# Kernel optimization log

Measured on AMD Instinct MI355X. Metric: run time of the kernel, lower is better.

The kernel has to match this reference:

```python
import jax, jax.numpy as jnp
import numpy as np

T, B, D_IN, NHID = 4096, 8, 512, 512

def setup_inputs() -> dict:
    key = jax.random.key(0)
    k1, k2, k3 = jax.random.split(key, 3)
    scale_i = 1.0 / np.sqrt(D_IN)
    scale_h = 1.0 / np.sqrt(NHID)
    x = jax.random.normal(k1, (T, B, D_IN), dtype=jnp.float32)
    hidden0 = jnp.zeros((2, B, NHID), dtype=jnp.float32)  # [h; cell]
    Wi = jax.random.normal(k2, (D_IN, 4 * NHID), dtype=jnp.float32) * scale_i
    bi = jnp.zeros((4 * NHID,), dtype=jnp.float32)
    Wh = jax.random.normal(k3, (NHID, 4 * NHID), dtype=jnp.float32) * scale_h
    bh = jnp.zeros((4 * NHID,), dtype=jnp.float32)
    return {"x": x, "hidden0": hidden0, "Wi": Wi, "bi": bi, "Wh": Wh, "bh": bh}

def reference(x, hidden0, Wi, bi, Wh, bh):
    n = Wh.shape[0]

    def update(state, xt):
        h, cell = state[0], state[1]               # [B, n] each
        pre = xt @ Wi + bi + h @ Wh + bh           # [B, 4n]
        gates = jax.nn.sigmoid(pre[:, : 3 * n])
        forget_gate = gates[:, :n]
        input_gate = gates[:, n : 2 * n]
        output_gate = gates[:, 2 * n : 3 * n]
        new_cell = jnp.tanh(pre[:, 3 * n :])
        cell = forget_gate * cell + input_gate * new_cell
        h = output_gate * jnp.tanh(cell)
        return jnp.stack([h, cell]), h

    new_state, hidden_stacked = jax.lax.scan(update, hidden0, x)
    return hidden_stacked, new_state
```

## Files before the change

### kernel.cpp

```cpp
#include <hip/hip_runtime.h>
#include <hip/hip_bf16.h>

#define T_STEPS 4096
#define BATCH 8
#define DIN 512
#define NH 512
#define G4 2048
#define NWV 32
#define JPW 16

typedef __attribute__((ext_vector_type(8))) short bf16x8;
typedef __attribute__((ext_vector_type(4))) float f32x4;
typedef __attribute__((ext_vector_type(4))) int i32x4;

__device__ __forceinline__ unsigned short f2b(float f) {
  __hip_bfloat16 h = __float2bfloat16(f);
  return __builtin_bit_cast(unsigned short, h);
}
__device__ __forceinline__ float b2f(unsigned short u) {
  unsigned int x = ((unsigned int)u) << 16;
  return __builtin_bit_cast(float, x);
}
__device__ __forceinline__ float sigf(float x) { return 1.f / (1.f + __expf(-x)); }
__device__ __forceinline__ float tanh_fast(float x) { return 1.f - 2.f / (1.f + __expf(2.f * x)); }

__global__ __launch_bounds__(512) void init_ws(const float* __restrict__ h0,
                                               unsigned int* __restrict__ tags,
                                               unsigned short* __restrict__ hbuf) {
  int tid = threadIdx.x;
  if (tid < NWV) tags[tid] = 0u;
  for (int i = tid; i < 4096; i += 512) {
    int b = i >> 9, j = i & 511;
    hbuf[i] = f2b(h0[b * NH + j]);
    hbuf[4096 + i] = 0;
  }
}

#define BM 64
#define BN 64
#define BK 16
__global__ __launch_bounds__(256) void xi_gemm(const float* __restrict__ x,
                                               const float* __restrict__ Wi,
                                               const float* __restrict__ bi,
                                               const float* __restrict__ bh,
                                               unsigned short* __restrict__ xi) {
  __shared__ float As[BK][BM + 4];
  __shared__ float Bs[BK][BN + 4];
  const int tid = threadIdx.x;
  const int m0 = blockIdx.x * BM;
  const int n0 = blockIdx.y * BN;
  const int tx = tid & 15, ty = tid >> 4;
  const int arow = tid & 63, ak = (tid >> 6) << 2;
  const int bk = tid >> 4, bn = (tid & 15) << 2;
  float acc[4][4] = {};
  for (int k0 = 0; k0 < DIN; k0 += BK) {
    float4 av = *(const float4*)(x + (size_t)(m0 + arow) * DIN + k0 + ak);
    float4 bv = *(const float4*)(Wi + (size_t)(k0 + bk) * G4 + n0 + bn);
    __syncthreads();
    As[ak + 0][arow] = av.x;
    As[ak + 1][arow] = av.y;
    As[ak + 2][arow] = av.z;
    As[ak + 3][arow] = av.w;
    *(float4*)&Bs[bk][bn] = bv;
    __syncthreads();
#pragma unroll
    for (int kk = 0; kk < BK; ++kk) {
      float am[4], bw[4];
      *(float4*)am = *(const float4*)&As[kk][ty << 2];
      *(float4*)bw = *(const float4*)&Bs[kk][tx << 2];
#pragma unroll
      for (int i = 0; i < 4; ++i)
#pragma unroll
        for (int j = 0; j < 4; ++j) acc[i][j] = fmaf(am[i], bw[j], acc[i][j]);
    }
  }
  const int m_base = m0 + (ty << 2);
  const int n_base = n0 + (tx << 2);
  const int tt = m_base >> 3;
  const int rg = (m_base & 7) >> 2;
  const int gate = n_base >> 9;
  const int wv = (n_base & 511) >> 4;
  const int col0 = n_base & 15;
#pragma unroll
  for (int j = 0; j < 4; ++j) {
    int n = n_base + j;
    float bs = bi[n] + bh[n];
    unsigned long long pk = 0;
#pragma unroll
    for (int i = 0; i < 4; ++i)
      pk |= (unsigned long long)f2b(acc[i][j] + bs) << (16 * i);
    int lane = rg * 16 + col0 + j;
    size_t u16idx = (((size_t)tt * NWV + wv) * 32 + lane) * 16 + gate * 4;
    *(unsigned long long*)(xi + u16idx) = pk;
  }
}

__global__ __launch_bounds__(64, 1) void lstm_rec(const float* __restrict__ Wh,
                                                  const float* __restrict__ h0c0,
                                                  const unsigned short* __restrict__ xi,
                                                  float* __restrict__ out,
                                                  unsigned int* tags,
                                                  unsigned short* hbuf) {
  const int wv = blockIdx.x;
  const int j0 = wv * JPW;
  const int lane = threadIdx.x;
  const int col = lane & 15;
  const int rg = lane >> 4;

  __shared__ bf16x8 bwS[4][16][64];

  {
    const int gp = lane >> 4, cp = lane & 15;
    const float* wsrc = Wh + (size_t)gp * NH + j0 + cp;
#pragma unroll 4
    for (int k = 0; k < 512; ++k) {
      float wval = wsrc[(size_t)k * G4];
      const int ks = k >> 5, kq = (k >> 3) & 3, e = k & 7;
      ((unsigned short*)&bwS[gp][ks][kq * 16 + cp])[e] = f2b(wval);
    }
  }
  __syncthreads();

  bf16x8 bwR0[16], bwR1[16];
#pragma unroll
  for (int ks = 0; ks < 16; ++ks) {
    bwR0[ks] = bwS[0][ks][lane];
    bwR1[ks] = bwS[1][ks][lane];
  }

  f32x4 cell = {0.f, 0.f, 0.f, 0.f};
  if (lane < 32) {
#pragma unroll
    for (int q = 0; q < 4; ++q)
      cell[q] = h0c0[(size_t)(BATCH + rg * 4 + q) * NH + j0 + col];
  }

  i32x4 xiC0, xiC1, xiN0, xiN1;
  {
    const unsigned short* xp = xi + ((size_t)wv * 32 + (lane & 31)) * 16;
    asm volatile("global_load_dwordx4 %0, %1, off" : "=&v"(xiC0) : "v"(xp));
    asm volatile("global_load_dwordx4 %0, %1, off offset:16" : "=&v"(xiC1) : "v"(xp));
  }
  f32x4 hq = {0.f, 0.f, 0.f, 0.f};

  const unsigned int* tp = tags + (lane & 31);
  unsigned int* myTag = tags + wv;

  for (int t = 0; t < T_STEPS; ++t) {
    {
      unsigned int tv;
      do {
        asm volatile("global_load_dword %0, %1, off sc1\n\ts_waitcnt vmcnt(0)"
                     : "=v"(tv) : "v"(tp) : "memory");
      } while (__any((int)tv < t));
    }

    const unsigned short* mb = hbuf + ((t & 1) << 12);
    const unsigned short* ap = mb + (col & 7) * 512 + (rg << 3);
    i32x4 afr[16];
    asm volatile("global_load_dwordx4 %0, %1, off sc1" : "=v"(afr[0]) : "v"(ap));
    asm volatile("global_load_dwordx4 %0, %1, off offset:64 sc1" : "=v"(afr[1]) : "v"(ap));
    asm volatile("global_load_dwordx4 %0, %1, off offset:128 sc1" : "=v"(afr[2]) : "v"(ap));
    asm volatile("global_load_dwordx4 %0, %1, off offset:192 sc1" : "=v"(afr[3]) : "v"(ap));
    asm volatile("global_load_dwordx4 %0, %1, off offset:256 sc1" : "=v"(afr[4]) : "v"(ap));
    asm volatile("global_load_dwordx4 %0, %1, off offset:320 sc1" : "=v"(afr[5]) : "v"(ap));
    asm volatile("global_load_dwordx4 %0, %1, off offset:384 sc1" : "=v"(afr[6]) : "v"(ap));
    asm volatile("global_load_dwordx4 %0, %1, off offset:448 sc1" : "=v"(afr[7]) : "v"(ap));
    asm volatile("global_load_dwordx4 %0, %1, off offset:512 sc1" : "=v"(afr[8]) : "v"(ap));
    asm volatile("global_load_dwordx4 %0, %1, off offset:576 sc1" : "=v"(afr[9]) : "v"(ap));
    asm volatile("global_load_dwordx4 %0, %1, off offset:640 sc1" : "=v"(afr[10]) : "v"(ap));
    asm volatile("global_load_dwordx4 %0, %1, off offset:704 sc1" : "=v"(afr[11]) : "v"(ap));
    asm volatile("global_load_dwordx4 %0, %1, off offset:768 sc1" : "=v"(afr[12]) : "v"(ap));
    asm volatile("global_load_dwordx4 %0, %1, off offset:832 sc1" : "=v"(afr[13]) : "v"(ap));
    asm volatile("global_load_dwordx4 %0, %1, off offset:896 sc1" : "=v"(afr[14]) : "v"(ap));
    asm volatile("global_load_dwordx4 %0, %1, off offset:960 sc1" : "=v"(afr[15]) : "v"(ap));
    asm volatile("s_waitcnt vmcnt(0)" ::: "memory");
    __builtin_amdgcn_sched_barrier(0);

    f32x4 acc[4][2];
    {
      unsigned int wrd[8] = {(unsigned int)xiC0[0], (unsigned int)xiC0[1],
                             (unsigned int)xiC0[2], (unsigned int)xiC0[3],
                             (unsigned int)xiC1[0], (unsigned int)xiC1[1],
                             (unsigned int)xiC1[2], (unsigned int)xiC1[3]};
      f32x4 z = {0.f, 0.f, 0.f, 0.f};
#pragma unroll
      for (int g = 0; g < 4; ++g) {
#pragma unroll
        for (int q = 0; q < 4; ++q) {
          const int idx = g * 4 + q;
          acc[g][0][q] = b2f((unsigned short)(wrd[idx >> 1] >> ((idx & 1) * 16)));
        }
        acc[g][1] = z;
      }
    }
#pragma unroll
    for (int ks = 0; ks < 16; ++ks) {
      bf16x8 a = __builtin_bit_cast(bf16x8, afr[ks]);
      acc[0][ks & 1] = __builtin_amdgcn_mfma_f32_16x16x32_bf16(a, bwR0[ks], acc[0][ks & 1], 0, 0, 0);
      acc[1][ks & 1] = __builtin_amdgcn_mfma_f32_16x16x32_bf16(a, bwR1[ks], acc[1][ks & 1], 0, 0, 0);
      acc[2][ks & 1] = __builtin_amdgcn_mfma_f32_16x16x32_bf16(a, bwS[2][ks][lane], acc[2][ks & 1], 0, 0, 0);
      acc[3][ks & 1] = __builtin_amdgcn_mfma_f32_16x16x32_bf16(a, bwS[3][ks][lane], acc[3][ks & 1], 0, 0, 0);
    }

#pragma unroll
    for (int q = 0; q < 4; ++q) {
      float pf = acc[0][0][q] + acc[0][1][q];
      float pi = acc[1][0][q] + acc[1][1][q];
      float po = acc[2][0][q] + acc[2][1][q];
      float pg = acc[3][0][q] + acc[3][1][q];
      float fg = sigf(pf), ig = sigf(pi), og = sigf(po), gg = tanh_fast(pg);
      float cn = fg * cell[q] + ig * gg;
      cell[q] = cn;
      hq[q] = og * tanh_fast(cn);
    }

    if (lane < 32) {
      unsigned short* pp = hbuf + (((t + 1) & 1) << 12) + (rg * 4) * 512 + j0 + col;
      unsigned int h0u = f2b(hq[0]), h1u = f2b(hq[1]), h2u = f2b(hq[2]), h3u = f2b(hq[3]);
      asm volatile("global_store_short %0, %1, off sc1" :: "v"(pp), "v"(h0u) : "memory");
      asm volatile("global_store_short %0, %1, off offset:1024 sc1" :: "v"(pp), "v"(h1u) : "memory");
      asm volatile("global_store_short %0, %1, off offset:2048 sc1" :: "v"(pp), "v"(h2u) : "memory");
      asm volatile("global_store_short %0, %1, off offset:3072 sc1" :: "v"(pp), "v"(h3u) : "memory");
    }
    asm volatile("s_waitcnt vmcnt(0)" ::: "memory");
    if (lane == 0) {
      unsigned int tn1 = (unsigned int)(t + 1);
      asm volatile("global_store_dword %0, %1, off sc1" :: "v"(myTag), "v"(tn1) : "memory");
    }

    if (lane < 32) {
#pragma unroll
      for (int q = 0; q < 4; ++q)
        out[((size_t)t * BATCH + (rg * 4 + q)) * NH + j0 + col] = hq[q];
    }
    {
      const int tn = (t + 1 < T_STEPS) ? (t + 1) : t;
      const unsigned short* xp = xi + (((size_t)tn * NWV + wv) * 32 + (lane & 31)) * 16;
      asm volatile("global_load_dwordx4 %0, %1, off" : "=&v"(xiN0) : "v"(xp));
      asm volatile("global_load_dwordx4 %0, %1, off offset:16" : "=&v"(xiN1) : "v"(xp));
    }
    xiC0 = xiN0;
    xiC1 = xiN1;
  }

  if (lane < 32) {
    const size_t tail = (size_t)T_STEPS * BATCH * NH;
#pragma unroll
    for (int q = 0; q < 4; ++q) {
      out[tail + (size_t)(rg * 4 + q) * NH + j0 + col] = hq[q];
      out[tail + (size_t)BATCH * NH + (size_t)(rg * 4 + q) * NH + j0 + col] = cell[q];
    }
  }
}

extern "C" void kernel_launch(void* const* d_in, const int* in_sizes, int n_in,
                              void* d_out, int out_size, void* d_ws, size_t ws_size,
                              hipStream_t stream) {
  const float* x  = (const float*)d_in[0];
  const float* h0 = (const float*)d_in[1];
  const float* Wi = (const float*)d_in[2];
  const float* bi = (const float*)d_in[3];
  const float* Wh = (const float*)d_in[4];
  const float* bh = (const float*)d_in[5];
  float* out = (float*)d_out;

  unsigned int* tags = (unsigned int*)d_ws;
  unsigned short* hbuf = (unsigned short*)((char*)d_ws + 256);
  unsigned short* xi = (unsigned short*)((char*)d_ws + 65536);

  init_ws<<<1, 512, 0, stream>>>(h0, tags, hbuf);
  dim3 g1((T_STEPS * BATCH) / BM, G4 / BN);
  xi_gemm<<<g1, 256, 0, stream>>>(x, Wi, bi, bh, xi);
  lstm_rec<<<NWV, 64, 0, stream>>>(Wh, h0, xi, out, tags, hbuf);
}
```

Before: 15.11 ms.

## Pipeline tag polling and overlap h-fragment loads with MFMA chunks

The spin-wait on per-wave step tags now keeps two loads in flight and waits with vmcnt(1), so each poll round trip overlaps the next. The accumulator init from precomputed input projections moves ahead of the h loads. The 16 h-fragment loads are consumed in four groups with staggered vmcnt waits, so MFMAs on the first fragments start while later loads are still arriving. This targets per-step latency on the serial recurrence, at the cost of more outstanding polling traffic and a slightly later view of tag updates.

```diff
diff --git a/kernel.cpp b/kernel.cpp
--- a/kernel.cpp
+++ b/kernel.cpp
@@ -148,11 +148,38 @@
 
   for (int t = 0; t < T_STEPS; ++t) {
     {
-      unsigned int tv;
-      do {
-        asm volatile("global_load_dword %0, %1, off sc1\n\ts_waitcnt vmcnt(0)"
-                     : "=v"(tv) : "v"(tp) : "memory");
-      } while (__any((int)tv < t));
+      unsigned int tvA, tvB;
+      asm volatile("global_load_dword %0, %1, off sc1" : "=&v"(tvA) : "v"(tp) : "memory");
+      for (;;) {
+        asm volatile("global_load_dword %0, %1, off sc1" : "=&v"(tvB) : "v"(tp) : "memory");
+        asm volatile("s_waitcnt vmcnt(1)" ::: "memory");
+        __builtin_amdgcn_sched_barrier(0);
+        if (__all((int)tvA >= t)) break;
+        asm volatile("global_load_dword %0, %1, off sc1" : "=&v"(tvA) : "v"(tp) : "memory");
+        asm volatile("s_waitcnt vmcnt(1)" ::: "memory");
+        __builtin_amdgcn_sched_barrier(0);
+        if (__all((int)tvB >= t)) break;
+      }
+      asm volatile("s_waitcnt vmcnt(0)" ::: "memory");
+      __builtin_amdgcn_sched_barrier(0);
+    }
+
+    f32x4 acc[4][2];
+    {
+      unsigned int wrd[8] = {(unsigned int)xiC0[0], (unsigned int)xiC0[1],
+                             (unsigned int)xiC0[2], (unsigned int)xiC0[3],
+                             (unsigned int)xiC1[0], (unsigned int)xiC1[1],
+                             (unsigned int)xiC1[2], (unsigned int)xiC1[3]};
+      f32x4 z = {0.f, 0.f, 0.f, 0.f};
+#pragma unroll
+      for (int g = 0; g < 4; ++g) {
+#pragma unroll
+        for (int q = 0; q < 4; ++q) {
+          const int idx = g * 4 + q;
+          acc[g][0][q] = b2f((unsigned short)(wrd[idx >> 1] >> ((idx & 1) * 16)));
+        }
+        acc[g][1] = z;
+      }
     }
 
     const unsigned short* mb = hbuf + ((t & 1) << 12);
@@ -174,34 +201,28 @@
     asm volatile("global_load_dwordx4 %0, %1, off offset:832 sc1" : "=v"(afr[13]) : "v"(ap));
     asm volatile("global_load_dwordx4 %0, %1, off offset:896 sc1" : "=v"(afr[14]) : "v"(ap));
     asm volatile("global_load_dwordx4 %0, %1, off offset:960 sc1" : "=v"(afr[15]) : "v"(ap));
+
+#define MFMA4(ks)                                                                          \
+    {                                                                                      \
+      bf16x8 a = __builtin_bit_cast(bf16x8, afr[ks]);                                      \
+      acc[0][(ks) & 1] = __builtin_amdgcn_mfma_f32_16x16x32_bf16(a, bwR0[ks], acc[0][(ks) & 1], 0, 0, 0); \
+      acc[1][(ks) & 1] = __builtin_amdgcn_mfma_f32_16x16x32_bf16(a, bwR1[ks], acc[1][(ks) & 1], 0, 0, 0); \
+      acc[2][(ks) & 1] = __builtin_amdgcn_mfma_f32_16x16x32_bf16(a, bwS[2][ks][lane], acc[2][(ks) & 1], 0, 0, 0); \
+      acc[3][(ks) & 1] = __builtin_amdgcn_mfma_f32_16x16x32_bf16(a, bwS[3][ks][lane], acc[3][(ks) & 1], 0, 0, 0); \
+    }
+    asm volatile("s_waitcnt vmcnt(12)" ::: "memory");
+    __builtin_amdgcn_sched_barrier(0);
+    MFMA4(0) MFMA4(1) MFMA4(2) MFMA4(3)
+    asm volatile("s_waitcnt vmcnt(8)" ::: "memory");
+    __builtin_amdgcn_sched_barrier(0);
+    MFMA4(4) MFMA4(5) MFMA4(6) MFMA4(7)
+    asm volatile("s_waitcnt vmcnt(4)" ::: "memory");
+    __builtin_amdgcn_sched_barrier(0);
+    MFMA4(8) MFMA4(9) MFMA4(10) MFMA4(11)
     asm volatile("s_waitcnt vmcnt(0)" ::: "memory");
     __builtin_amdgcn_sched_barrier(0);
-
-    f32x4 acc[4][2];
-    {
-      unsigned int wrd[8] = {(unsigned int)xiC0[0], (unsigned int)xiC0[1],
-                             (unsigned int)xiC0[2], (unsigned int)xiC0[3],
-                             (unsigned int)xiC1[0], (unsigned int)xiC1[1],
-                             (unsigned int)xiC1[2], (unsigned int)xiC1[3]};
-      f32x4 z = {0.f, 0.f, 0.f, 0.f};
-#pragma unroll
-      for (int g = 0; g < 4; ++g) {
-#pragma unroll
-        for (int q = 0; q < 4; ++q) {
-          const int idx = g * 4 + q;
-          acc[g][0][q] = b2f((unsigned short)(wrd[idx >> 1] >> ((idx & 1) * 16)));
-        }
-        acc[g][1] = z;
-      }
-    }
-#pragma unroll
-    for (int ks = 0; ks < 16; ++ks) {
-      bf16x8 a = __builtin_bit_cast(bf16x8, afr[ks]);
-      acc[0][ks & 1] = __builtin_amdgcn_mfma_f32_16x16x32_bf16(a, bwR0[ks], acc[0][ks & 1], 0, 0, 0);
-      acc[1][ks & 1] = __builtin_amdgcn_mfma_f32_16x16x32_bf16(a, bwR1[ks], acc[1][ks & 1], 0, 0, 0);
-      acc[2][ks & 1] = __builtin_amdgcn_mfma_f32_16x16x32_bf16(a, bwS[2][ks][lane], acc[2][ks & 1], 0, 0, 0);
-      acc[3][ks & 1] = __builtin_amdgcn_mfma_f32_16x16x32_bf16(a, bwS[3][ks][lane], acc[3][ks & 1], 0, 0, 0);
-    }
+    MFMA4(12) MFMA4(13) MFMA4(14) MFMA4(15)
+#undef MFMA4
 
 #pragma unroll
     for (int q = 0; q < 4; ++q) {
```

Measured after the change: 14.04 ms, median of 2. 7.1% less time.
